# Performance work log

Measured on AMD Instinct MI355X. Metric: run time of the kernel, lower is better.

The kernel has to match this reference:

```python
import jax, jax.numpy as jnp
import numpy as np

N, E = 50000, 600000
DIN, D, C = 239, 128, 2
NEG_SLOPE_MLP = 0.01   # nn.LeakyReLU default
NEG_SLOPE_ATT = 0.2    # GATConv default


def leaky(x, s):
    return jnp.where(x >= 0, x, s * x)


def setup_inputs() -> dict:
    key = jax.random.key(0)
    ks = jax.random.split(key, 12)
    sc = lambda d: 1.0 / np.sqrt(d)
    return {
        "x": jax.random.normal(ks[0], (N, DIN), jnp.float32),
        "edge_index": jax.random.randint(ks[1], (2, E), 0, N, jnp.int32),
        "edge_type": jax.random.randint(ks[2], (E,), 0, 4, jnp.int32),
        "W_in": jax.random.normal(ks[3], (DIN, D), jnp.float32) * sc(DIN),
        "b_in": jnp.zeros((D,), jnp.float32),
        "W_gat": jax.random.normal(ks[4], (D, D), jnp.float32) * sc(D),
        "att_src": jax.random.normal(ks[5], (D,), jnp.float32) * sc(D),
        "att_dst": jax.random.normal(ks[6], (D,), jnp.float32) * sc(D),
        "b_gat": jnp.zeros((D,), jnp.float32),
        "W_h": jax.random.normal(ks[7], (D, D), jnp.float32) * sc(D),
        "b_h": jnp.zeros((D,), jnp.float32),
        "W_out": jax.random.normal(ks[8], (D, C), jnp.float32) * sc(D),
        "b_out": jnp.zeros((C,), jnp.float32),
    }


def reference(x, edge_index, edge_type, W_in, b_in, W_gat, att_src, att_dst,
              b_gat, W_h, b_h, W_out, b_out):
    # input encoder: Linear + LeakyReLU
    h = leaky(x @ W_in + b_in, NEG_SLOPE_MLP)                      # [N, D]

    # GATConv (heads=1): add self loops, edge attention, segment softmax over dst
    loops = jnp.arange(N, dtype=edge_index.dtype)
    src = jnp.concatenate([edge_index[0], loops])                  # [E+N]
    dst = jnp.concatenate([edge_index[1], loops])

    g = h @ W_gat                                                  # [N, D]
    a_src = g @ att_src                                            # [N]
    a_dst = g @ att_dst                                            # [N]
    e = leaky(a_src[src] + a_dst[dst], NEG_SLOPE_ATT)              # [E+N]

    m = jax.ops.segment_max(e, dst, num_segments=N)                # self-loops => no empty segs
    w = jnp.exp(e - m[dst])
    z = jax.ops.segment_sum(w, dst, num_segments=N)
    alpha = w / z[dst]                                             # [E+N]

    out = jax.ops.segment_sum(alpha[:, None] * g[src], dst, num_segments=N) + b_gat

    # dropout is identity in eval mode
    h2 = leaky(out @ W_h + b_h, NEG_SLOPE_MLP)
    return h2 @ W_out + b_out                                      # [N, C]
```

## Files before the change

kernel.cpp:

```cpp
#include <hip/hip_runtime.h>

#define NNODE 50000
#define NEDGE 600000
#define KDIN  239
#define DDIM  128
#define NTILES 3125
#define NBG   782
#define NBUCK 256
#define BSZ   196
#define NPB   128
#define CHP   4688

typedef _Float16 half8 __attribute__((ext_vector_type(8)));
typedef _Float16 half4 __attribute__((ext_vector_type(4)));
typedef __attribute__((ext_vector_type(4))) float f32x4;

__device__ __forceinline__ ushort f2h(float f){
  union { _Float16 h; ushort u; } c; c.h = (_Float16)f; return c.u;
}

__global__ __launch_bounds__(256) void pre_k(
    const float* __restrict__ W_in, const float* __restrict__ W_gat, const float* __restrict__ W_h,
    ushort* __restrict__ BfA, ushort* __restrict__ BfB, ushort* __restrict__ BfC,
    const int* __restrict__ ei, int* __restrict__ cpart)
{
  __shared__ int hb[NBUCK];
  const int b = blockIdx.x, t = threadIdx.x;
  if (b < NPB){
    hb[t] = 0;
    __syncthreads();
    const int e0 = b*CHP, e1 = min(NEDGE, e0+CHP);
    for (int e=e0+t; e<e1; e+=256){
      int dst = min(max(ei[NEDGE+e],0), NNODE-1);
      atomicAdd(&hb[dst/BSZ], 1);
    }
    __syncthreads();
    cpart[b*NBUCK + t] = hb[t];
  } else if (b < NPB + 128){
    int idx = (b-NPB)*256 + t; int n = idx >> 8, k = idx & 255;
    BfA[idx] = (k < KDIN) ? f2h(W_in[(size_t)k*DDIM + n]) : (ushort)0;
  } else if (b < NPB + 192){
    int idx = (b-NPB-128)*256 + t; int n = idx >> 7, k = idx & 127;
    BfB[idx] = f2h(W_gat[(size_t)k*DDIM + n]);
  } else {
    int idx = (b-NPB-192)*256 + t; int n = idx >> 7, k = idx & 127;
    BfC[idx] = f2h(W_h[(size_t)k*DDIM + n]);
  }
}

template<int KSTEPS, int EPI, int XW, int AMODE>
__global__ __launch_bounds__(256, 4) void gemm8_k(
    const float* __restrict__ Afp, const ushort* __restrict__ Af,
    const ushort* __restrict__ Btf, const float* __restrict__ bias,
    float* __restrict__ outf, ushort* __restrict__ outh,
    const float* __restrict__ vs, const float* __restrict__ vd,
    float* __restrict__ os, float* __restrict__ od,
    float* __restrict__ bms, float* __restrict__ bmd,
    const int* __restrict__ ei, int* __restrict__ cpart, int* __restrict__ pairs)
{
  constexpr int Kpad = KSTEPS*32;
  constexpr int Kb   = Kpad*2;
  if (XW == 1 && blockIdx.x >= NBG){
    __shared__ int sc[NBUCK];
    const int t = threadIdx.x;
    int tot = 0;
    #pragma unroll 8
    for (int i=0;i<NPB;i++) tot += cpart[i*NBUCK + t];
    sc[t] = tot;
    __syncthreads();
    #pragma unroll
    for (int off=1; off<NBUCK; off<<=1){
      int v = (t>=off) ? sc[t-off] : 0;
      __syncthreads();
      sc[t] += v;
      __syncthreads();
    }
    int run = sc[t] - tot;
    #pragma unroll 8
    for (int i=0;i<NPB;i++){
      int c = cpart[i*NBUCK + t];
      cpart[i*NBUCK + t] = run;
      run += c;
    }
    return;
  }
  if (XW == 2 && blockIdx.x >= NBG){
    __shared__ int cur[NBUCK];
    const int pb = blockIdx.x - NBG;
    cur[threadIdx.x] = cpart[pb*NBUCK + threadIdx.x];
    __syncthreads();
    const int e0 = pb*CHP, e1 = min(NEDGE, e0+CHP);
    for (int e=e0+threadIdx.x; e<e1; e+=256){
      int dst = min(max(ei[NEDGE+e],0), NNODE-1);
      int src = min(max(ei[e],0), NNODE-1);
      int bk = (unsigned)dst / BSZ;
      int pos = atomicAdd(&cur[bk], 1);
      pairs[pos] = src | ((dst - bk*BSZ) << 16);
    }
    return;
  }
  __shared__ __attribute__((aligned(16))) ushort Bs[128*Kpad];
  {
    constexpr int CH = (128*Kb)/16;
    #pragma unroll
    for (int it=0; it<CH/256; ++it){
      const int idx = it*256 + threadIdx.x;
      const int row = (idx*16)/Kb, sl = (idx*16)%Kb;
      const half8 v = *(const half8*)(Btf + (size_t)idx*8);
      *(half8*)((char*)Bs + row*Kb + (sl ^ ((row&7)<<4))) = v;
    }
  }
  __syncthreads();
  const int lane = threadIdx.x & 63;
  const int wave = threadIdx.x >> 6;
  const int q = lane >> 4, c = lane & 15;
  const int tile = blockIdx.x*4 + wave;
  if (tile >= NTILES) return;
  const int rowBase = tile*16;
  const int arow = rowBase + c;
  half8 af[KSTEPS];
  if (AMODE == 0){
    const float* __restrict__ ap = Afp + (size_t)arow*KDIN;
    #pragma unroll
    for (int s=0;s<KSTEPS-1;s++){
      const float* __restrict__ p = ap + s*32 + q*8;
      #pragma unroll
      for (int i=0;i<8;i++) af[s][i] = (_Float16)p[i];
    }
    {
      const int s = KSTEPS-1;
      #pragma unroll
      for (int i=0;i<8;i++){
        const int k = s*32 + q*8 + i;
        af[s][i] = (_Float16)((k < KDIN) ? ap[k] : 0.f);
      }
    }
  } else {
    const ushort* __restrict__ ap = Af + (size_t)arow*Kpad + q*8;
    #pragma unroll
    for (int s=0;s<KSTEPS;s++) af[s] = *(const half8*)(ap + s*32);
  }
  f32x4 acc[8];
  #pragma unroll
  for (int t=0;t<8;t++) acc[t] = (f32x4){0.f,0.f,0.f,0.f};
  const int swz = (c&7)<<4;
  const char* __restrict__ bsl = (const char*)Bs + c*Kb;
  #pragma unroll
  for (int s=0;s<KSTEPS;s++){
    const int so = (s*64 + q*16) ^ swz;
    #pragma unroll
    for (int t=0;t<8;t++){
      const half8 bf = *(const half8*)(bsl + t*16*Kb + so);
      acc[t] = __builtin_amdgcn_mfma_f32_16x16x32_f16(af[s], bf, acc[t], 0,0,0);
    }
  }
  float pr0[4] = {0,0,0,0}, pr1[4] = {0,0,0,0};
  #pragma unroll
  for (int t=0;t<8;t++){
    const int col = 16*t + c;
    const float bv = (EPI != 1) ? bias[col] : 0.f;
    float va=0.f, vb=0.f;
    if (EPI == 1){ va = vs[col]; vb = vd[col]; }
    if (EPI == 2){ va = vs[2*col]; vb = vs[2*col+1]; }
    #pragma unroll
    for (int r=0;r<4;r++){
      const int row = rowBase + q*4 + r;
      float v = acc[t][r] + bv;
      if (EPI != 1) v = (v >= 0.f) ? v : 0.01f*v;
      if (EPI == 0){
        outh[(size_t)row*DDIM + col] = f2h(v);
      } else if (EPI == 1){
        outh[(size_t)row*DDIM + col] = f2h(v);
        pr0[r] += v*va; pr1[r] += v*vb;
      } else {
        pr0[r] += v*va; pr1[r] += v*vb;
      }
    }
  }
  if (EPI >= 1){
    float lmax_s = -3.0e38f, lmax_d = -3.0e38f;
    #pragma unroll
    for (int r=0;r<4;r++){
      float s0 = pr0[r], s1 = pr1[r];
      s0 += __shfl_xor(s0,8); s1 += __shfl_xor(s1,8);
      s0 += __shfl_xor(s0,4); s1 += __shfl_xor(s1,4);
      s0 += __shfl_xor(s0,2); s1 += __shfl_xor(s1,2);
      s0 += __shfl_xor(s0,1); s1 += __shfl_xor(s1,1);
      if (EPI == 1){ lmax_s = fmaxf(lmax_s, s0); lmax_d = fmaxf(lmax_d, s1); }
      if (c == 0){
        const int row = rowBase + q*4 + r;
        if (EPI == 1){ os[row] = s0; od[row] = s1; }
        else { float2 y2; y2.x = s0 + vd[0]; y2.y = s1 + vd[1];
               *(float2*)&outf[(size_t)row*2] = y2; }
      }
    }
    if (EPI == 1){
      #pragma unroll
      for (int off=32; off>0; off>>=1){
        lmax_s = fmaxf(lmax_s, __shfl_xor(lmax_s, off));
        lmax_d = fmaxf(lmax_d, __shfl_xor(lmax_d, off));
      }
      if (lane == 0){ bms[tile] = lmax_s; bmd[tile] = lmax_d; }
    }
  }
}

__global__ __launch_bounds__(256) void fine_k(const int* __restrict__ pairs,
    const int* __restrict__ cpart, int* __restrict__ offs, int* __restrict__ degv,
    int* __restrict__ es, const float* __restrict__ bms, const float* __restrict__ bmd,
    float* __restrict__ gmf)
{
  __shared__ int fh[256];
  __shared__ int sc[256];
  const int b = blockIdx.x, t = threadIdx.x;
  if (b == NBUCK){
    float ms = -3.0e38f, md = -3.0e38f;
    for (int i=t; i<NTILES; i+=256){ ms = fmaxf(ms, bms[i]); md = fmaxf(md, bmd[i]); }
    #pragma unroll
    for (int off=32; off>0; off>>=1){
      ms = fmaxf(ms, __shfl_xor(ms, off));
      md = fmaxf(md, __shfl_xor(md, off));
    }
    float* red = (float*)fh;
    const int w = t >> 6;
    if ((t & 63) == 0){ red[w] = ms; red[4+w] = md; }
    __syncthreads();
    if (t == 0){
      gmf[0] = fmaxf(fmaxf(red[0],red[1]), fmaxf(red[2],red[3]));
      gmf[1] = fmaxf(fmaxf(red[4],red[5]), fmaxf(red[6],red[7]));
    }
    return;
  }
  const int s0 = cpart[b];
  const int s1 = (b < NBUCK-1) ? cpart[b+1] : NEDGE;
  fh[t] = 0;
  __syncthreads();
  for (int i=s0+t; i<s1; i+=256)
    atomicAdd(&fh[pairs[i] >> 16], 1);
  __syncthreads();
  const int deg = fh[t];
  sc[t] = deg;
  __syncthreads();
  #pragma unroll
  for (int off=1; off<256; off<<=1){
    int v = (t>=off) ? sc[t-off] : 0;
    __syncthreads();
    sc[t] += v;
    __syncthreads();
  }
  const int excl = sc[t] - deg;
  const int dst = b*BSZ + t;
  if (t < BSZ && dst < NNODE){ offs[dst] = s0 + excl; degv[dst] = deg; }
  fh[t] = s0 + excl;
  __syncthreads();
  for (int i=s0+t; i<s1; i+=256){
    const int p = pairs[i];
    const int pos = atomicAdd(&fh[p >> 16], 1);
    es[pos] = p & 0xFFFF;
  }
}

__global__ __launch_bounds__(256) void agg_k(const ushort* __restrict__ gf,
    const int* __restrict__ offs, const int* __restrict__ degv,
    const int* __restrict__ es,
    const float* __restrict__ a_src, const float* __restrict__ a_dst,
    const float* __restrict__ gmf, const float* __restrict__ b_gat,
    ushort* __restrict__ og)
{
  const int lane = threadIdx.x & 63;
  const int half = lane >> 5, li = lane & 31;
  const int dst = blockIdx.x*8 + (threadIdx.x >> 6)*2 + half;
  if (dst >= NNODE) return;
  float M = gmf[0] + gmf[1];
  M = (M >= 0.f) ? M : 0.2f*M;
  const int start = offs[dst];
  const int deg = degv[dst];
  const int* __restrict__ bin = es + start;
  const float ad = a_dst[dst];
  f32x4 a0={0,0,0,0}, a1={0,0,0,0}, a2={0,0,0,0}, a3={0,0,0,0};
  float w0s=0.f, w1s=0.f, w2s=0.f, w3s=0.f;
  int j = 0;
  for (; j+3 < deg; j += 4){
    const int i0=bin[j], i1=bin[j+1], i2=bin[j+2], i3=bin[j+3];
    float e0=a_src[i0]+ad; e0=(e0>=0.f)?e0:0.2f*e0;
    float e1=a_src[i1]+ad; e1=(e1>=0.f)?e1:0.2f*e1;
    float e2=a_src[i2]+ad; e2=(e2>=0.f)?e2:0.2f*e2;
    float e3=a_src[i3]+ad; e3=(e3>=0.f)?e3:0.2f*e3;
    const float w0=__expf(e0-M), w1=__expf(e1-M), w2=__expf(e2-M), w3=__expf(e3-M);
    const half4 g0 = *(const half4*)(gf + (size_t)i0*DDIM + li*4);
    const half4 g1 = *(const half4*)(gf + (size_t)i1*DDIM + li*4);
    const half4 g2 = *(const half4*)(gf + (size_t)i2*DDIM + li*4);
    const half4 g3 = *(const half4*)(gf + (size_t)i3*DDIM + li*4);
    #pragma unroll
    for (int i=0;i<4;i++){
      a0[i] += w0*(float)g0[i]; a1[i] += w1*(float)g1[i];
      a2[i] += w2*(float)g2[i]; a3[i] += w3*(float)g3[i];
    }
    w0s += w0; w1s += w1; w2s += w2; w3s += w3;
  }
  for (; j < deg; ++j){
    const int si = bin[j];
    float e0=a_src[si]+ad; e0=(e0>=0.f)?e0:0.2f*e0;
    const float w = __expf(e0-M);
    const half4 gv = *(const half4*)(gf + (size_t)si*DDIM + li*4);
    #pragma unroll
    for (int i=0;i<4;i++) a0[i] += w*(float)gv[i];
    w0s += w;
  }
  {
    float evs=a_src[dst]+ad; evs=(evs>=0.f)?evs:0.2f*evs;
    const float w = __expf(evs-M);
    const half4 gv = *(const half4*)(gf + (size_t)dst*DDIM + li*4);
    #pragma unroll
    for (int i=0;i<4;i++) a0[i] += w*(float)gv[i];
    w0s += w;
  }
  const float inv = 1.f/(w0s+w1s+w2s+w3s);
  const float4 bg = *(const float4*)&b_gat[li*4];
  ushort4 o;
  o.x = f2h((a0[0]+a1[0]+a2[0]+a3[0])*inv + bg.x);
  o.y = f2h((a0[1]+a1[1]+a2[1]+a3[1])*inv + bg.y);
  o.z = f2h((a0[2]+a1[2]+a2[2]+a3[2])*inv + bg.z);
  o.w = f2h((a0[3]+a1[3]+a2[3]+a3[3])*inv + bg.w);
  *(ushort4*)(og + (size_t)dst*DDIM + li*4) = o;
}

extern "C" void kernel_launch(void* const* d_in, const int* in_sizes, int n_in,
                              void* d_out, int out_size, void* d_ws, size_t ws_size,
                              hipStream_t stream)
{
  const float* x       = (const float*)d_in[0];
  const int*   ei      = (const int*)d_in[1];
  const float* W_in    = (const float*)d_in[3];
  const float* b_in    = (const float*)d_in[4];
  const float* W_gat   = (const float*)d_in[5];
  const float* att_src = (const float*)d_in[6];
  const float* att_dst = (const float*)d_in[7];
  const float* b_gat   = (const float*)d_in[8];
  const float* W_h     = (const float*)d_in[9];
  const float* b_h     = (const float*)d_in[10];
  const float* W_out   = (const float*)d_in[11];
  const float* b_out   = (const float*)d_in[12];

  char* ws = (char*)d_ws;
  ushort*   hf     = (ushort*)  (ws + 0);
  ushort*   gf     = (ushort*)  (ws + 12800000);
  ushort*   og     = (ushort*)  (ws + 25600000);
  ushort*   BfA    = (ushort*)  (ws + 38400000);
  ushort*   BfB    = (ushort*)  (ws + 38600000);
  ushort*   BfC    = (ushort*)  (ws + 38700000);
  int*      cpart  = (int*)     (ws + 38800000);
  int*      pairs  = (int*)     (ws + 39100000);
  int*      es     = (int*)     (ws + 41500000);
  int*      offs   = (int*)     (ws + 43900000);
  int*      degv   = (int*)     (ws + 44100000);
  float*    a_src  = (float*)   (ws + 44300000);
  float*    a_dst  = (float*)   (ws + 44500000);
  float*    gm     = (float*)   (ws + 44700000);
  float*    bmaxS  = (float*)   (ws + 44700032);
  float*    bmaxD  = (float*)   (ws + 44712544);

  pre_k<<<NPB + 256, 256, 0, stream>>>(W_in, W_gat, W_h, BfA, BfB, BfC, ei, cpart);
  gemm8_k<8,0,1,0><<<NBG + 1, 256, 0, stream>>>(x, nullptr, BfA, b_in,
      nullptr, hf, nullptr, nullptr, nullptr, nullptr, nullptr, nullptr, nullptr, cpart, nullptr);
  gemm8_k<4,1,2,1><<<NBG + NPB, 256, 0, stream>>>(nullptr, hf, BfB, nullptr,
      nullptr, gf, att_src, att_dst, a_src, a_dst, bmaxS, bmaxD, ei, cpart, pairs);
  fine_k<<<NBUCK + 1, 256, 0, stream>>>(pairs, cpart, offs, degv, es, bmaxS, bmaxD, gm);
  agg_k<<<6250, 256, 0, stream>>>(gf, offs, degv, es, a_src, a_dst, gm, b_gat, og);
  gemm8_k<4,2,0,1><<<NBG, 256, 0, stream>>>(nullptr, og, BfC, b_h,
      (float*)d_out, nullptr, W_out, b_out, nullptr, nullptr, nullptr, nullptr, nullptr, nullptr, nullptr);
}
```

Before: 181.4 us.

## Fuse input-encoder GEMM with GAT projection GEMM via LDS-staged intermediate

Merges the x@W_in GEMM and the h@W_gat GEMM into one kernel. The 16x128 half-precision h tile stays in shared memory per wave, so h no longer makes a round trip through global memory. The bucket prefix scan moves into its own single-block launch, and the scatter blocks ride alongside the fused GEMM. The fused kernel uses about 80KB of LDS with launch bounds of 2 blocks, which lowers occupancy, and it adds an extra launch for the scan.

```diff
diff --git a/kernel.cpp b/kernel.cpp
--- a/kernel.cpp
+++ b/kernel.cpp
@@ -48,45 +48,45 @@
   }
 }
 
-template<int KSTEPS, int EPI, int XW, int AMODE>
-__global__ __launch_bounds__(256, 4) void gemm8_k(
-    const float* __restrict__ Afp, const ushort* __restrict__ Af,
-    const ushort* __restrict__ Btf, const float* __restrict__ bias,
-    float* __restrict__ outf, ushort* __restrict__ outh,
+__global__ __launch_bounds__(256) void scan_k(int* __restrict__ cpart)
+{
+  __shared__ int sc[NBUCK];
+  const int t = threadIdx.x;
+  int tot = 0;
+  #pragma unroll 8
+  for (int i=0;i<NPB;i++) tot += cpart[i*NBUCK + t];
+  sc[t] = tot;
+  __syncthreads();
+  #pragma unroll
+  for (int off=1; off<NBUCK; off<<=1){
+    int v = (t>=off) ? sc[t-off] : 0;
+    __syncthreads();
+    sc[t] += v;
+    __syncthreads();
+  }
+  int run = sc[t] - tot;
+  #pragma unroll 8
+  for (int i=0;i<NPB;i++){
+    int c = cpart[i*NBUCK + t];
+    cpart[i*NBUCK + t] = run;
+    run += c;
+  }
+}
+
+__global__ __launch_bounds__(256, 2) void gemmAB_k(
+    const float* __restrict__ x, const ushort* __restrict__ BfA,
+    const ushort* __restrict__ BfB, const float* __restrict__ b_in,
+    ushort* __restrict__ gf,
     const float* __restrict__ vs, const float* __restrict__ vd,
     float* __restrict__ os, float* __restrict__ od,
     float* __restrict__ bms, float* __restrict__ bmd,
-    const int* __restrict__ ei, int* __restrict__ cpart, int* __restrict__ pairs)
-{
-  constexpr int Kpad = KSTEPS*32;
-  constexpr int Kb   = Kpad*2;
-  if (XW == 1 && blockIdx.x >= NBG){
-    __shared__ int sc[NBUCK];
-    const int t = threadIdx.x;
-    int tot = 0;
-    #pragma unroll 8
-    for (int i=0;i<NPB;i++) tot += cpart[i*NBUCK + t];
-    sc[t] = tot;
-    __syncthreads();
-    #pragma unroll
-    for (int off=1; off<NBUCK; off<<=1){
-      int v = (t>=off) ? sc[t-off] : 0;
-      __syncthreads();
-      sc[t] += v;
-      __syncthreads();
-    }
-    int run = sc[t] - tot;
-    #pragma unroll 8
-    for (int i=0;i<NPB;i++){
-      int c = cpart[i*NBUCK + t];
-      cpart[i*NBUCK + t] = run;
-      run += c;
-    }
-    return;
-  }
-  if (XW == 2 && blockIdx.x >= NBG){
-    __shared__ int cur[NBUCK];
-    const int pb = blockIdx.x - NBG;
+    const int* __restrict__ ei, const int* __restrict__ cpart, int* __restrict__ pairs)
+{
+  __shared__ __attribute__((aligned(16))) ushort Bs[128*256];
+  __shared__ __attribute__((aligned(16))) ushort ht[4][16*128];
+  if (blockIdx.x < NPB){
+    int* cur = (int*)Bs;
+    const int pb = blockIdx.x;
     cur[threadIdx.x] = cpart[pb*NBUCK + threadIdx.x];
     __syncthreads();
     const int e0 = pb*CHP, e1 = min(NEDGE, e0+CHP);
@@ -99,16 +99,136 @@
     }
     return;
   }
+  #pragma unroll
+  for (int it=0; it<16; ++it){
+    const int idx = it*256 + threadIdx.x;
+    const int row = idx >> 5, sl = (idx & 31)*16;
+    const half8 v = *(const half8*)(BfA + (size_t)idx*8);
+    *(half8*)((char*)Bs + row*512 + (sl ^ ((row&7)<<4))) = v;
+  }
+  __syncthreads();
+  const int lane = threadIdx.x & 63;
+  const int wave = threadIdx.x >> 6;
+  const int q = lane >> 4, c = lane & 15;
+  const int tile = (blockIdx.x - NPB)*4 + wave;
+  const bool act = tile < NTILES;
+  const int rowBase = tile*16;
+  const int swz = (c&7)<<4;
+  f32x4 acc[8];
+  if (act){
+    const float* __restrict__ ap = x + (size_t)(rowBase + c)*KDIN;
+    half8 af[8];
+    #pragma unroll
+    for (int s=0;s<7;s++){
+      const float* __restrict__ p = ap + s*32 + q*8;
+      #pragma unroll
+      for (int i=0;i<8;i++) af[s][i] = (_Float16)p[i];
+    }
+    #pragma unroll
+    for (int i=0;i<8;i++){
+      const int k = 224 + q*8 + i;
+      af[7][i] = (_Float16)((k < KDIN) ? ap[k] : 0.f);
+    }
+    #pragma unroll
+    for (int t=0;t<8;t++) acc[t] = (f32x4){0.f,0.f,0.f,0.f};
+    const char* __restrict__ bsl = (const char*)Bs + c*512;
+    #pragma unroll
+    for (int s=0;s<8;s++){
+      const int so = (s*64 + q*16) ^ swz;
+      #pragma unroll
+      for (int t=0;t<8;t++){
+        const half8 bf = *(const half8*)(bsl + t*16*512 + so);
+        acc[t] = __builtin_amdgcn_mfma_f32_16x16x32_f16(af[s], bf, acc[t], 0,0,0);
+      }
+    }
+    char* __restrict__ hw = (char*)&ht[wave][0];
+    #pragma unroll
+    for (int t=0;t<8;t++){
+      const int col = 16*t + c;
+      const float bv = b_in[col];
+      #pragma unroll
+      for (int r=0;r<4;r++){
+        const int row = q*4 + r;
+        float v = acc[t][r] + bv;
+        v = (v >= 0.f) ? v : 0.01f*v;
+        *(_Float16*)(hw + ((row*256 + col*2) ^ ((row&7)<<4))) = (_Float16)v;
+      }
+    }
+  }
+  __syncthreads();
+  #pragma unroll
+  for (int it=0; it<8; ++it){
+    const int idx = it*256 + threadIdx.x;
+    const int row = idx >> 4, sl = (idx & 15)*16;
+    const half8 v = *(const half8*)(BfB + (size_t)idx*8);
+    *(half8*)((char*)Bs + row*256 + (sl ^ ((row&7)<<4))) = v;
+  }
+  __syncthreads();
+  if (!act) return;
+  half8 af2[4];
+  const char* __restrict__ hr = (const char*)&ht[wave][0] + c*256;
+  #pragma unroll
+  for (int s=0;s<4;s++) af2[s] = *(const half8*)(hr + ((s*64 + q*16) ^ swz));
+  #pragma unroll
+  for (int t=0;t<8;t++) acc[t] = (f32x4){0.f,0.f,0.f,0.f};
+  const char* __restrict__ bsl2 = (const char*)Bs + c*256;
+  #pragma unroll
+  for (int s=0;s<4;s++){
+    const int so = (s*64 + q*16) ^ swz;
+    #pragma unroll
+    for (int t=0;t<8;t++){
+      const half8 bf = *(const half8*)(bsl2 + t*16*256 + so);
+      acc[t] = __builtin_amdgcn_mfma_f32_16x16x32_f16(af2[s], bf, acc[t], 0,0,0);
+    }
+  }
+  float pr0[4] = {0,0,0,0}, pr1[4] = {0,0,0,0};
+  #pragma unroll
+  for (int t=0;t<8;t++){
+    const int col = 16*t + c;
+    const float va = vs[col], vb = vd[col];
+    #pragma unroll
+    for (int r=0;r<4;r++){
+      const int row = rowBase + q*4 + r;
+      const float v = acc[t][r];
+      gf[(size_t)row*DDIM + col] = f2h(v);
+      pr0[r] += v*va; pr1[r] += v*vb;
+    }
+  }
+  float lmax_s = -3.0e38f, lmax_d = -3.0e38f;
+  #pragma unroll
+  for (int r=0;r<4;r++){
+    float s0 = pr0[r], s1 = pr1[r];
+    s0 += __shfl_xor(s0,8); s1 += __shfl_xor(s1,8);
+    s0 += __shfl_xor(s0,4); s1 += __shfl_xor(s1,4);
+    s0 += __shfl_xor(s0,2); s1 += __shfl_xor(s1,2);
+    s0 += __shfl_xor(s0,1); s1 += __shfl_xor(s1,1);
+    lmax_s = fmaxf(lmax_s, s0); lmax_d = fmaxf(lmax_d, s1);
+    if (c == 0){
+      const int row = rowBase + q*4 + r;
+      os[row] = s0; od[row] = s1;
+    }
+  }
+  #pragma unroll
+  for (int off=32; off>0; off>>=1){
+    lmax_s = fmaxf(lmax_s, __shfl_xor(lmax_s, off));
+    lmax_d = fmaxf(lmax_d, __shfl_xor(lmax_d, off));
+  }
+  if (lane == 0){ bms[tile] = lmax_s; bmd[tile] = lmax_d; }
+}
+
+__global__ __launch_bounds__(256, 4) void gemmC_k(
+    const ushort* __restrict__ Af, const ushort* __restrict__ Btf,
+    const float* __restrict__ bias, float* __restrict__ outf,
+    const float* __restrict__ Wo, const float* __restrict__ bo)
+{
+  constexpr int Kpad = 128, Kb = 256;
   __shared__ __attribute__((aligned(16))) ushort Bs[128*Kpad];
-  {
-    constexpr int CH = (128*Kb)/16;
-    #pragma unroll
-    for (int it=0; it<CH/256; ++it){
-      const int idx = it*256 + threadIdx.x;
-      const int row = (idx*16)/Kb, sl = (idx*16)%Kb;
-      const half8 v = *(const half8*)(Btf + (size_t)idx*8);
-      *(half8*)((char*)Bs + row*Kb + (sl ^ ((row&7)<<4))) = v;
-    }
+  #pragma unroll
+  for (int it=0; it<8; ++it){
+    const int idx = it*256 + threadIdx.x;
+    const int row = idx >> 4, sl = (idx & 15)*16;
+    const half8 v = *(const half8*)(Btf + (size_t)idx*8);
+    *(half8*)((char*)Bs + row*Kb + (sl ^ ((row&7)<<4))) = v;
   }
   __syncthreads();
   const int lane = threadIdx.x & 63;
@@ -117,36 +237,17 @@
   const int tile = blockIdx.x*4 + wave;
   if (tile >= NTILES) return;
   const int rowBase = tile*16;
-  const int arow = rowBase + c;
-  half8 af[KSTEPS];
-  if (AMODE == 0){
-    const float* __restrict__ ap = Afp + (size_t)arow*KDIN;
-    #pragma unroll
-    for (int s=0;s<KSTEPS-1;s++){
-      const float* __restrict__ p = ap + s*32 + q*8;
-      #pragma unroll
-      for (int i=0;i<8;i++) af[s][i] = (_Float16)p[i];
-    }
-    {
-      const int s = KSTEPS-1;
-      #pragma unroll
-      for (int i=0;i<8;i++){
-        const int k = s*32 + q*8 + i;
-        af[s][i] = (_Float16)((k < KDIN) ? ap[k] : 0.f);
-      }
-    }
-  } else {
-    const ushort* __restrict__ ap = Af + (size_t)arow*Kpad + q*8;
-    #pragma unroll
-    for (int s=0;s<KSTEPS;s++) af[s] = *(const half8*)(ap + s*32);
-  }
+  half8 af[4];
+  const ushort* __restrict__ ap = Af + (size_t)(rowBase + c)*Kpad + q*8;
+  #pragma unroll
+  for (int s=0;s<4;s++) af[s] = *(const half8*)(ap + s*32);
   f32x4 acc[8];
   #pragma unroll
   for (int t=0;t<8;t++) acc[t] = (f32x4){0.f,0.f,0.f,0.f};
   const int swz = (c&7)<<4;
   const char* __restrict__ bsl = (const char*)Bs + c*Kb;
   #pragma unroll
-  for (int s=0;s<KSTEPS;s++){
+  for (int s=0;s<4;s++){
     const int so = (s*64 + q*16) ^ swz;
     #pragma unroll
     for (int t=0;t<8;t++){
@@ -158,49 +259,26 @@
   #pragma unroll
   for (int t=0;t<8;t++){
     const int col = 16*t + c;
-    const float bv = (EPI != 1) ? bias[col] : 0.f;
-    float va=0.f, vb=0.f;
-    if (EPI == 1){ va = vs[col]; vb = vd[col]; }
-    if (EPI == 2){ va = vs[2*col]; vb = vs[2*col+1]; }
+    const float bv = bias[col];
+    const float va = Wo[2*col], vb = Wo[2*col+1];
     #pragma unroll
     for (int r=0;r<4;r++){
+      float v = acc[t][r] + bv;
+      v = (v >= 0.f) ? v : 0.01f*v;
+      pr0[r] += v*va; pr1[r] += v*vb;
+    }
+  }
+  #pragma unroll
+  for (int r=0;r<4;r++){
+    float s0 = pr0[r], s1 = pr1[r];
+    s0 += __shfl_xor(s0,8); s1 += __shfl_xor(s1,8);
+    s0 += __shfl_xor(s0,4); s1 += __shfl_xor(s1,4);
+    s0 += __shfl_xor(s0,2); s1 += __shfl_xor(s1,2);
+    s0 += __shfl_xor(s0,1); s1 += __shfl_xor(s1,1);
+    if (c == 0){
       const int row = rowBase + q*4 + r;
-      float v = acc[t][r] + bv;
-      if (EPI != 1) v = (v >= 0.f) ? v : 0.01f*v;
-      if (EPI == 0){
-        outh[(size_t)row*DDIM + col] = f2h(v);
-      } else if (EPI == 1){
-        outh[(size_t)row*DDIM + col] = f2h(v);
-        pr0[r] += v*va; pr1[r] += v*vb;
-      } else {
-        pr0[r] += v*va; pr1[r] += v*vb;
-      }
-    }
-  }
-  if (EPI >= 1){
-    float lmax_s = -3.0e38f, lmax_d = -3.0e38f;
-    #pragma unroll
-    for (int r=0;r<4;r++){
-      float s0 = pr0[r], s1 = pr1[r];
-      s0 += __shfl_xor(s0,8); s1 += __shfl_xor(s1,8);
-      s0 += __shfl_xor(s0,4); s1 += __shfl_xor(s1,4);
-      s0 += __shfl_xor(s0,2); s1 += __shfl_xor(s1,2);
-      s0 += __shfl_xor(s0,1); s1 += __shfl_xor(s1,1);
-      if (EPI == 1){ lmax_s = fmaxf(lmax_s, s0); lmax_d = fmaxf(lmax_d, s1); }
-      if (c == 0){
-        const int row = rowBase + q*4 + r;
-        if (EPI == 1){ os[row] = s0; od[row] = s1; }
-        else { float2 y2; y2.x = s0 + vd[0]; y2.y = s1 + vd[1];
-               *(float2*)&outf[(size_t)row*2] = y2; }
-      }
-    }
-    if (EPI == 1){
-      #pragma unroll
-      for (int off=32; off>0; off>>=1){
-        lmax_s = fmaxf(lmax_s, __shfl_xor(lmax_s, off));
-        lmax_d = fmaxf(lmax_d, __shfl_xor(lmax_d, off));
-      }
-      if (lane == 0){ bms[tile] = lmax_s; bmd[tile] = lmax_d; }
+      float2 y2; y2.x = s0 + bo[0]; y2.y = s1 + bo[1];
+      *(float2*)&outf[(size_t)row*2] = y2;
     }
   }
 }
@@ -343,7 +421,6 @@
   const float* b_out   = (const float*)d_in[12];
 
   char* ws = (char*)d_ws;
-  ushort*   hf     = (ushort*)  (ws + 0);
   ushort*   gf     = (ushort*)  (ws + 12800000);
   ushort*   og     = (ushort*)  (ws + 25600000);
   ushort*   BfA    = (ushort*)  (ws + 38400000);
@@ -361,12 +438,10 @@
   float*    bmaxD  = (float*)   (ws + 44712544);
 
   pre_k<<<NPB + 256, 256, 0, stream>>>(W_in, W_gat, W_h, BfA, BfB, BfC, ei, cpart);
-  gemm8_k<8,0,1,0><<<NBG + 1, 256, 0, stream>>>(x, nullptr, BfA, b_in,
-      nullptr, hf, nullptr, nullptr, nullptr, nullptr, nullptr, nullptr, nullptr, cpart, nullptr);
-  gemm8_k<4,1,2,1><<<NBG + NPB, 256, 0, stream>>>(nullptr, hf, BfB, nullptr,
-      nullptr, gf, att_src, att_dst, a_src, a_dst, bmaxS, bmaxD, ei, cpart, pairs);
+  scan_k<<<1, 256, 0, stream>>>(cpart);
+  gemmAB_k<<<NPB + NBG, 256, 0, stream>>>(x, BfA, BfB, b_in, gf,
+      att_src, att_dst, a_src, a_dst, bmaxS, bmaxD, ei, cpart, pairs);
   fine_k<<<NBUCK + 1, 256, 0, stream>>>(pairs, cpart, offs, degv, es, bmaxS, bmaxD, gm);
   agg_k<<<6250, 256, 0, stream>>>(gf, offs, degv, es, a_src, a_dst, gm, b_gat, og);
-  gemm8_k<4,2,0,1><<<NBG, 256, 0, stream>>>(nullptr, og, BfC, b_h,
-      (float*)d_out, nullptr, W_out, b_out, nullptr, nullptr, nullptr, nullptr, nullptr, nullptr, nullptr);
-}
+  gemmC_k<<<NBG, 256, 0, stream>>>(og, BfC, b_h, (float*)d_out, W_out, b_out);
+}
```

New measurement: 183.3 us. No clear change (+1.0%).
